# Performance work log

Hardware: AMD Instinct MI355X
Metric: run time of the kernel (lower is better)

## Reference

```python
import jax, jax.numpy as jnp
import numpy as np

HEADS, OUT_CH = 8, 32  # GATConv(128, 256//8, heads=8) -> concat width 256
NEG_SLOPE = 0.2


def setup_inputs() -> dict:
    key = jax.random.key(0)
    ks = jax.random.split(key, 12)
    N, E, F_IN = 50000, 500000, 128
    H, C = HEADS, OUT_CH
    HID = H * C            # 256
    x = jax.random.normal(ks[0], (N, F_IN), dtype=jnp.float32)
    edge_index = jax.random.randint(ks[1], (2, E), 0, N, dtype=jnp.int64)
    s = 1.0 / np.sqrt(F_IN)
    W_gat = jax.random.normal(ks[2], (F_IN, H * C), dtype=jnp.float32) * s
    att_src = jax.random.normal(ks[3], (H, C), dtype=jnp.float32) * (1.0 / np.sqrt(C))
    att_dst = jax.random.normal(ks[4], (H, C), dtype=jnp.float32) * (1.0 / np.sqrt(C))
    b_gat = jnp.zeros((HID,), dtype=jnp.float32)
    W1 = jax.random.normal(ks[5], (HID, HID // 2), dtype=jnp.float32) * (1.0 / np.sqrt(HID))
    b1 = jnp.zeros((HID // 2,), dtype=jnp.float32)
    W2 = jax.random.normal(ks[6], (HID // 2, 6), dtype=jnp.float32) * (1.0 / np.sqrt(HID // 2))
    b2 = jnp.zeros((6,), dtype=jnp.float32)
    return {"x": x, "edge_index": edge_index, "W_gat": W_gat, "att_src": att_src,
            "att_dst": att_dst, "b_gat": b_gat, "W1": W1, "b1": b1, "W2": W2, "b2": b2}


def _gat_forward(x, edge_index, W_gat, att_src, att_dst, b_gat):
    N = x.shape[0]
    H, C = HEADS, OUT_CH
    # add self loops (PyG GATConv default)
    loop = jnp.arange(N, dtype=edge_index.dtype)
    src = jnp.concatenate([edge_index[0], loop])
    dst = jnp.concatenate([edge_index[1], loop])
    # per-node transform: [N, H, C]
    xh = (x @ W_gat).reshape(N, H, C)
    a_src = jnp.einsum('nhc,hc->nh', xh, att_src)  # [N, H]
    a_dst = jnp.einsum('nhc,hc->nh', xh, att_dst)  # [N, H]
    alpha = a_src[src] + a_dst[dst]                # [Etot, H]
    alpha = jnp.where(alpha >= 0, alpha, NEG_SLOPE * alpha)  # leaky relu
    # segment softmax over destination nodes
    m = jax.ops.segment_max(alpha, dst, num_segments=N)     # [N, H]
    m = jax.lax.stop_gradient(m)
    ex = jnp.exp(alpha - m[dst])
    denom = jax.ops.segment_sum(ex, dst, num_segments=N)    # [N, H]
    coef = ex / denom[dst]                                   # [Etot, H]
    # weighted scatter-add aggregation
    msgs = xh[src] * coef[:, :, None]                        # [Etot, H, C]
    out = jax.ops.segment_sum(msgs, dst, num_segments=N)     # [N, H, C]
    return out.reshape(N, H * C) + b_gat


def reference(x, edge_index, W_gat, att_src, att_dst, b_gat, W1, b1, W2, b2):
    h = _gat_forward(x, edge_index, W_gat, att_src, att_dst, b_gat)
    h = jax.nn.elu(h)
    g = jnp.mean(h, axis=0, keepdims=True)   # [1, 256] mean pool
    g = jax.nn.relu(g @ W1 + b1)
    return g @ W2 + b2                        # [1, 6] logits
```

## Files before the change

kernel.cpp:

```cpp
#include <hip/hip_runtime.h>
#include <hip/hip_fp8.h>
#include <math.h>

#define F_IN 128
#define HID 256
#define NH 8
#define CAP 40
#define BCAP 4096

typedef _Float16 h16;
typedef __attribute__((ext_vector_type(8))) _Float16 half8;
typedef __attribute__((ext_vector_type(4))) float f32x4;

__device__ inline unsigned char f32_to_fp8(float v) {
#if __has_builtin(__builtin_amdgcn_cvt_pk_fp8_f32)
    return (unsigned char)(__builtin_amdgcn_cvt_pk_fp8_f32(v, v, 0, false) & 0xff);
#else
    __hip_fp8_e4m3 t(v);
    return (unsigned char)t.__x;
#endif
}

__device__ inline void fp8x4_to_f32(int w, float* out) {
#if __has_builtin(__builtin_amdgcn_cvt_pk_f32_fp8)
    auto lo = __builtin_amdgcn_cvt_pk_f32_fp8(w, false);
    auto hi = __builtin_amdgcn_cvt_pk_f32_fp8(w, true);
    out[0] = lo[0]; out[1] = lo[1]; out[2] = hi[0]; out[3] = hi[1];
#else
    #pragma unroll
    for (int k = 0; k < 4; ++k) {
        __hip_fp8_e4m3 t;
        t.__x = (unsigned char)((w >> (8 * k)) & 0xff);
        out[k] = (float)t;
    }
#endif
}

__global__ void k_prep(const float* __restrict__ Wg, h16* __restrict__ Wt_sw,
                       int* gcur, float* g2, int n) {
    int i = blockIdx.x * 256 + threadIdx.x;
    if (i < 256) gcur[i] = 0;
    if (i < 256 * HID) g2[i] = 0.f;
    if (i < 4096) {
        int fid = i;
        int lane16 = fid & 15;
        int quad = (fid >> 4) & 3;
        int ks = (fid >> 6) & 3;
        int ct = fid >> 8;
        int col = ct * 16 + lane16;
        int k0 = ks * 32 + quad * 8;
        half8 v;
        #pragma unroll
        for (int j = 0; j < 8; ++j) v[j] = (h16)Wg[(size_t)(k0 + j) * HID + col];
        *(half8*)(Wt_sw + (size_t)fid * 8) = v;
    }
}

__global__ __launch_bounds__(256) void k_part(const int* __restrict__ dstp,
                                              const int* __restrict__ srcp,
                                              unsigned int* __restrict__ gbuck,
                                              int* __restrict__ gcur,
                                              int e, int nbuck) {
    __shared__ int hist[256];
    __shared__ int base[256];
    __shared__ int cur[256];
    int t = threadIdx.x;
    int c0 = blockIdx.x * 4096;
    hist[t] = 0;
    __syncthreads();
    #pragma unroll
    for (int j = 0; j < 16; ++j) {
        int i = c0 + j * 256 + t;
        if (i < e) atomicAdd(&hist[dstp[i] >> 8], 1);
    }
    __syncthreads();
    if (t < nbuck && hist[t] > 0) base[t] = atomicAdd(&gcur[t], hist[t]);
    cur[t] = 0;
    __syncthreads();
    #pragma unroll
    for (int j = 0; j < 16; ++j) {
        int i = c0 + j * 256 + t;
        if (i < e) {
            int d = dstp[i];
            int b = d >> 8;
            int pos = base[b] + atomicAdd(&cur[b], 1);
            if (pos < BCAP)
                gbuck[(size_t)b * BCAP + pos] =
                    ((unsigned)(d & 255) << 16) | (unsigned)srcp[i];
        }
    }
}

__global__ __launch_bounds__(256) void k_bin(const unsigned int* __restrict__ gbuck,
                                             const int* __restrict__ gcur,
                                             int* __restrict__ cnt,
                                             unsigned short* __restrict__ bin,
                                             int n, int nbuck) {
    __shared__ int hist[256];
    __shared__ int cur[256];
    __shared__ __align__(16) unsigned short bl[256 * CAP];
    int t = threadIdx.x;
    int b = blockIdx.x;
    int count = gcur[b];
    if (count > BCAP) count = BCAP;
    hist[t] = 0;
    __syncthreads();
    const unsigned int* bb = gbuck + (size_t)b * BCAP;
    for (int j = t; j < count; j += 256) atomicAdd(&hist[(bb[j] >> 16) & 255], 1);
    __syncthreads();
    int node = b * 256 + t;
    if (node < n) {
        int hh = hist[t];
        cnt[node] = hh > CAP ? CAP : hh;
    }
    cur[t] = 0;
    __syncthreads();
    for (int j = t; j < count; j += 256) {
        unsigned int wv = bb[j];
        int dl = (wv >> 16) & 255;
        int pos = atomicAdd(&cur[dl], 1);
        if (pos < CAP) bl[dl * CAP + pos] = (unsigned short)(wv & 0xffff);
    }
    __syncthreads();
    const int4* s4 = (const int4*)bl;
    int4* d4 = (int4*)(bin + (size_t)b * 256 * CAP);
    #pragma unroll
    for (int q = 0; q < 5; ++q) d4[q * 256 + t] = s4[q * 256 + t];
}

__global__ __launch_bounds__(512) void k_gemm(const float* __restrict__ x,
                                              const h16* __restrict__ Wt_sw,
                                              const float* __restrict__ att_s,
                                              const float* __restrict__ att_d,
                                              unsigned char* __restrict__ xh8,
                                              float* __restrict__ a_src,
                                              float* __restrict__ a_dst,
                                              int n, int ntiles) {
    __shared__ h16 wlds[32768];
    int t = threadIdx.x;
    int w = t >> 6, l = t & 63;
    int lane16 = l & 15, quad = l >> 4;

    float4 pv0[4], pv1[4];
    int tile = blockIdx.x * 8 + w;
    bool have = tile < ntiles;
    int row0 = tile * 16;
    if (have) {
        int rA = row0 + lane16;
        if (rA >= n) rA = n - 1;
        const float* xrow = x + (size_t)rA * F_IN + quad * 8;
        #pragma unroll
        for (int ks = 0; ks < 4; ++ks) {
            pv0[ks] = *(const float4*)(xrow + ks * 32);
            pv1[ks] = *(const float4*)(xrow + ks * 32 + 4);
        }
    }
    {
        const int4* wsrc = (const int4*)Wt_sw;
        int4* wdst = (int4*)wlds;
        #pragma unroll
        for (int i = 0; i < 8; ++i) wdst[i * 512 + t] = wsrc[i * 512 + t];
    }
    __syncthreads();
    if (!have) return;
    const h16* wl = wlds + (size_t)l * 8;

    half8 afr[4];
    #pragma unroll
    for (int ks = 0; ks < 4; ++ks) {
        half8 a;
        a[0] = (h16)pv0[ks].x; a[1] = (h16)pv0[ks].y;
        a[2] = (h16)pv0[ks].z; a[3] = (h16)pv0[ks].w;
        a[4] = (h16)pv1[ks].x; a[5] = (h16)pv1[ks].y;
        a[6] = (h16)pv1[ks].z; a[7] = (h16)pv1[ks].w;
        afr[ks] = a;
    }
    f32x4 acc[16];
    #pragma unroll
    for (int ct = 0; ct < 16; ++ct) acc[ct] = (f32x4){0.f, 0.f, 0.f, 0.f};
    #pragma unroll
    for (int ct = 0; ct < 16; ++ct) {
        #pragma unroll
        for (int ks = 0; ks < 4; ++ks) {
            half8 bfr = *(const half8*)(wl + (ct * 4 + ks) * 512);
            acc[ct] = __builtin_amdgcn_mfma_f32_16x16x32_f16(afr[ks], bfr, acc[ct], 0, 0, 0);
        }
    }
    if (row0 + 16 <= n) {
        #pragma unroll
        for (int ct = 0; ct < 16; ++ct) {
            int col = ct * 16 + lane16;
            #pragma unroll
            for (int r = 0; r < 4; ++r)
                xh8[(size_t)(row0 + quad * 4 + r) * HID + col] = f32_to_fp8(acc[ct][r]);
        }
    } else {
        #pragma unroll
        for (int ct = 0; ct < 16; ++ct) {
            int col = ct * 16 + lane16;
            #pragma unroll
            for (int r = 0; r < 4; ++r) {
                int row = row0 + quad * 4 + r;
                if (row < n) xh8[(size_t)row * HID + col] = f32_to_fp8(acc[ct][r]);
            }
        }
    }
    #pragma unroll
    for (int h = 0; h < 8; ++h) {
        float ps[4] = {0.f, 0.f, 0.f, 0.f};
        float pd[4] = {0.f, 0.f, 0.f, 0.f};
        #pragma unroll
        for (int cc = 0; cc < 2; ++cc) {
            int ct = h * 2 + cc;
            float as_ = att_s[ct * 16 + lane16];
            float ad_ = att_d[ct * 16 + lane16];
            #pragma unroll
            for (int r = 0; r < 4; ++r) {
                ps[r] += acc[ct][r] * as_;
                pd[r] += acc[ct][r] * ad_;
            }
        }
        #pragma unroll
        for (int m = 1; m < 16; m <<= 1) {
            #pragma unroll
            for (int r = 0; r < 4; ++r) {
                ps[r] += __shfl_xor(ps[r], m, 64);
                pd[r] += __shfl_xor(pd[r], m, 64);
            }
        }
        if (lane16 == 0) {
            #pragma unroll
            for (int r = 0; r < 4; ++r) {
                int row = row0 + quad * 4 + r;
                if (row < n) {
                    a_src[row * NH + h] = ps[r];
                    a_dst[row * NH + h] = pd[r];
                }
            }
        }
    }
}

__global__ __launch_bounds__(256) void k_agg(const unsigned char* __restrict__ xh8,
                                             const float* __restrict__ a_src,
                                             const float* __restrict__ a_dst,
                                             const int* __restrict__ cnt,
                                             const unsigned short* __restrict__ bin,
                                             const float* __restrict__ b_gat,
                                             float* __restrict__ g2, int n) {
    __shared__ float wpart[4][260];
    int t = threadIdx.x;
    int slot = t >> 4;
    int cl = t & 15;
    int c0 = cl * 16;
    int h = cl >> 1;
    int nn = blockIdx.x * 16 + slot;
    bool alive = nn < n;
    int nnc = alive ? nn : (n - 1);

    float ad = a_dst[nnc * NH + h];
    int deg = cnt[nnc];
    if (deg > CAP) deg = CAP;

    float al = a_src[nnc * NH + h] + ad;
    al = al > 0.f ? al : 0.2f * al;
    float ex = __expf(al);
    float den = ex;
    float acc[16];
    {
        int4 v = *(const int4*)(xh8 + (size_t)nnc * HID + c0);
        float f[16];
        fp8x4_to_f32(v.x, f); fp8x4_to_f32(v.y, f + 4);
        fp8x4_to_f32(v.z, f + 8); fp8x4_to_f32(v.w, f + 12);
        #pragma unroll
        for (int i = 0; i < 16; ++i) acc[i] = ex * f[i];
    }
    const unsigned short* brow = bin + (size_t)nnc * CAP;
    int j = 0;
    for (; j + 4 <= deg; j += 4) {
        ushort4 ss = *(const ushort4*)(brow + j);
        int s0 = ss.x, s1 = ss.y, s2 = ss.z, s3 = ss.w;
        float aa[4];
        aa[0] = a_src[s0 * NH + h];
        aa[1] = a_src[s1 * NH + h];
        aa[2] = a_src[s2 * NH + h];
        aa[3] = a_src[s3 * NH + h];
        int4 v0 = *(const int4*)(xh8 + (size_t)s0 * HID + c0);
        int4 v1 = *(const int4*)(xh8 + (size_t)s1 * HID + c0);
        int4 v2 = *(const int4*)(xh8 + (size_t)s2 * HID + c0);
        int4 v3 = *(const int4*)(xh8 + (size_t)s3 * HID + c0);
        float e4[4];
        #pragma unroll
        for (int q = 0; q < 4; ++q) {
            float a2 = aa[q] + ad;
            a2 = a2 > 0.f ? a2 : 0.2f * a2;
            e4[q] = __expf(a2);
            den += e4[q];
        }
        float f[16];
        fp8x4_to_f32(v0.x, f); fp8x4_to_f32(v0.y, f + 4);
        fp8x4_to_f32(v0.z, f + 8); fp8x4_to_f32(v0.w, f + 12);
        #pragma unroll
        for (int i = 0; i < 16; ++i) acc[i] += e4[0] * f[i];
        fp8x4_to_f32(v1.x, f); fp8x4_to_f32(v1.y, f + 4);
        fp8x4_to_f32(v1.z, f + 8); fp8x4_to_f32(v1.w, f + 12);
        #pragma unroll
        for (int i = 0; i < 16; ++i) acc[i] += e4[1] * f[i];
        fp8x4_to_f32(v2.x, f); fp8x4_to_f32(v2.y, f + 4);
        fp8x4_to_f32(v2.z, f + 8); fp8x4_to_f32(v2.w, f + 12);
        #pragma unroll
        for (int i = 0; i < 16; ++i) acc[i] += e4[2] * f[i];
        fp8x4_to_f32(v3.x, f); fp8x4_to_f32(v3.y, f + 4);
        fp8x4_to_f32(v3.z, f + 8); fp8x4_to_f32(v3.w, f + 12);
        #pragma unroll
        for (int i = 0; i < 16; ++i) acc[i] += e4[3] * f[i];
    }
    for (; j < deg; ++j) {
        int s = brow[j];
        float a2 = a_src[s * NH + h] + ad;
        a2 = a2 > 0.f ? a2 : 0.2f * a2;
        float e2 = __expf(a2);
        den += e2;
        int4 v = *(const int4*)(xh8 + (size_t)s * HID + c0);
        float f[16];
        fp8x4_to_f32(v.x, f); fp8x4_to_f32(v.y, f + 4);
        fp8x4_to_f32(v.z, f + 8); fp8x4_to_f32(v.w, f + 12);
        #pragma unroll
        for (int i = 0; i < 16; ++i) acc[i] += e2 * f[i];
    }
    float inv = 1.f / den;
    float val[16];
    #pragma unroll
    for (int q = 0; q < 4; ++q) {
        float4 bv = *(const float4*)(b_gat + c0 + q * 4);
        val[q * 4 + 0] = acc[q * 4 + 0] * inv + bv.x;
        val[q * 4 + 1] = acc[q * 4 + 1] * inv + bv.y;
        val[q * 4 + 2] = acc[q * 4 + 2] * inv + bv.z;
        val[q * 4 + 3] = acc[q * 4 + 3] * inv + bv.w;
    }
    #pragma unroll
    for (int i = 0; i < 16; ++i) {
        float v = val[i];
        v = v > 0.f ? v : expm1f(v);
        val[i] = alive ? v : 0.f;
    }
    #pragma unroll
    for (int i = 0; i < 16; ++i) {
        val[i] += __shfl_xor(val[i], 16, 64);
        val[i] += __shfl_xor(val[i], 32, 64);
    }
    int w = t >> 6, lw = t & 63;
    if (lw < 16) {
        #pragma unroll
        for (int q = 0; q < 4; ++q)
            *(f32x4*)(&wpart[w][c0 + q * 4]) =
                (f32x4){val[q * 4], val[q * 4 + 1], val[q * 4 + 2], val[q * 4 + 3]};
    }
    __syncthreads();
    float s = wpart[0][t] + wpart[1][t] + wpart[2][t] + wpart[3][t];
    atomicAdd(&g2[(blockIdx.x & 255) * HID + t], s);
}

__global__ __launch_bounds__(256) void k_mlp(const float* __restrict__ g2,
                                             const float* __restrict__ W1,
                                             const float* __restrict__ b1,
                                             const float* __restrict__ W2,
                                             const float* __restrict__ b2,
                                             float* __restrict__ out, int n) {
    __shared__ float gm[HID];
    __shared__ float h1p[2][128];
    __shared__ float h1[128];
    int t = threadIdx.x;
    float s = 0.f;
    for (int b = 0; b < 256; ++b) s += g2[b * HID + t];
    gm[t] = s / (float)n;
    __syncthreads();
    int o = t & 127, hf = t >> 7;
    float a = 0.f;
    #pragma unroll 4
    for (int k = hf * 128; k < hf * 128 + 128; ++k) a += gm[k] * W1[k * 128 + o];
    h1p[hf][o] = a;
    __syncthreads();
    if (t < 128) {
        float v = h1p[0][t] + h1p[1][t] + b1[t];
        h1[t] = v > 0.f ? v : 0.f;
    }
    __syncthreads();
    if (t < 6) {
        float a2 = b2[t];
        for (int k = 0; k < 128; ++k) a2 += h1[k] * W2[k * 6 + t];
        out[t] = a2;
    }
}

extern "C" void kernel_launch(void* const* d_in, const int* in_sizes, int n_in,
                              void* d_out, int out_size, void* d_ws, size_t ws_size,
                              hipStream_t stream) {
    const float* x     = (const float*)d_in[0];
    const int*   ei    = (const int*)d_in[1];
    const float* Wg    = (const float*)d_in[2];
    const float* att_s = (const float*)d_in[3];
    const float* att_d = (const float*)d_in[4];
    const float* b_gat = (const float*)d_in[5];
    const float* W1    = (const float*)d_in[6];
    const float* b1    = (const float*)d_in[7];
    const float* W2    = (const float*)d_in[8];
    const float* b2    = (const float*)d_in[9];

    int N = in_sizes[0] / F_IN;
    int E = in_sizes[1] / 2;
    const int* srcp = ei;
    const int* dstp = ei + E;
    int nblk = (N + 15) / 16;
    int ntiles = (N + 15) / 16;
    int nbuck = (N + 255) >> 8;

    char* ws = (char*)d_ws;
    size_t off = 0;
    auto alloc = [&](size_t bytes) {
        size_t o = off;
        off += (bytes + 255) & ~(size_t)255;
        return o;
    };
    unsigned char* xh8 = (unsigned char*)(ws + alloc((size_t)N * HID));
    h16*   Wt      = (h16*)(ws + alloc((size_t)F_IN * HID * 2));
    float* asr     = (float*)(ws + alloc((size_t)N * NH * 4));
    float* ads     = (float*)(ws + alloc((size_t)N * NH * 4));
    int*   cnt     = (int*)(ws + alloc((size_t)N * 4));
    unsigned short* bin = (unsigned short*)(ws + alloc((size_t)nbuck * 256 * CAP * 2));
    float* g2      = (float*)(ws + alloc((size_t)256 * HID * 4));
    unsigned int* gbuck = (unsigned int*)(ws + alloc((size_t)nbuck * BCAP * 4));
    int*   gcur    = (int*)(ws + alloc((size_t)256 * 4));

    int nb1 = (E + 4095) / 4096;
    int ngemm = (ntiles + 7) / 8;

    k_prep<<<256, 256, 0, stream>>>(Wg, Wt, gcur, g2, N);
    k_part<<<nb1, 256, 0, stream>>>(dstp, srcp, gbuck, gcur, E, nbuck);
    k_bin<<<nbuck, 256, 0, stream>>>(gbuck, gcur, cnt, bin, N, nbuck);
    k_gemm<<<ngemm, 512, 0, stream>>>(x, Wt, att_s, att_d, xh8, asr, ads, N, ntiles);
    k_agg<<<nblk, 256, 0, stream>>>(xh8, asr, ads, cnt, bin, b_gat, g2, N);
    k_mlp<<<1, 256, 0, stream>>>(g2, W1, b1, W2, b2, (float*)d_out, N);
}
```

Measured before the change: 188.7 us.

## Merge edge partition and node GEMM into one launch, locally sort edges per bucket

Replaces the separate partition and GEMM kernels with a single launch whose first blocks partition edges and whose remaining blocks run the MFMA GEMM. The two independent stages can then overlap, and one kernel launch and its tail are removed. The partition path also sorts each chunk by bucket in shared memory, using a prefix scan, before writing, so global bucket writes become contiguous runs instead of scattered stores. The cost is 64KB of LDS per block for both roles, which may lower occupancy for the partition blocks, plus extra barriers for the scan.

```diff
diff --git a/kernel.cpp b/kernel.cpp
--- a/kernel.cpp
+++ b/kernel.cpp
@@ -56,37 +56,185 @@
     }
 }
 
-__global__ __launch_bounds__(256) void k_part(const int* __restrict__ dstp,
-                                              const int* __restrict__ srcp,
-                                              unsigned int* __restrict__ gbuck,
-                                              int* __restrict__ gcur,
-                                              int e, int nbuck) {
-    __shared__ int hist[256];
-    __shared__ int base[256];
-    __shared__ int cur[256];
+__global__ __launch_bounds__(512) void k_ga(const float* __restrict__ x,
+                                            const h16* __restrict__ Wt_sw,
+                                            const float* __restrict__ att_s,
+                                            const float* __restrict__ att_d,
+                                            const int* __restrict__ dstp,
+                                            const int* __restrict__ srcp,
+                                            unsigned char* __restrict__ xh8,
+                                            float* __restrict__ a_src,
+                                            float* __restrict__ a_dst,
+                                            unsigned int* __restrict__ gbuck,
+                                            int* __restrict__ gcur,
+                                            int n, int e, int ntiles,
+                                            int nbuck, int npart) {
+    __shared__ __align__(16) char smem[65536];
     int t = threadIdx.x;
-    int c0 = blockIdx.x * 4096;
-    hist[t] = 0;
-    __syncthreads();
-    #pragma unroll
-    for (int j = 0; j < 16; ++j) {
-        int i = c0 + j * 256 + t;
-        if (i < e) atomicAdd(&hist[dstp[i] >> 8], 1);
-    }
-    __syncthreads();
-    if (t < nbuck && hist[t] > 0) base[t] = atomicAdd(&gcur[t], hist[t]);
-    cur[t] = 0;
-    __syncthreads();
-    #pragma unroll
-    for (int j = 0; j < 16; ++j) {
-        int i = c0 + j * 256 + t;
-        if (i < e) {
-            int d = dstp[i];
-            int b = d >> 8;
-            int pos = base[b] + atomicAdd(&cur[b], 1);
-            if (pos < BCAP)
-                gbuck[(size_t)b * BCAP + pos] =
-                    ((unsigned)(d & 255) << 16) | (unsigned)srcp[i];
+
+    if (blockIdx.x < (unsigned)npart) {
+        int* hist  = (int*)smem;
+        int* scn   = hist + 256;
+        int* lbase = scn + 256;
+        int* lcur  = lbase + 256;
+        int* base  = lcur + 256;
+        unsigned int* sorted = (unsigned int*)(base + 256);
+        int c0 = blockIdx.x * 4096;
+
+        if (t < 256) hist[t] = 0;
+        __syncthreads();
+
+        unsigned int w8[8];
+        int b8[8];
+        #pragma unroll
+        for (int k = 0; k < 8; ++k) {
+            int i = c0 + k * 512 + t;
+            if (i < e) {
+                int d = dstp[i];
+                int s = srcp[i];
+                int b = d >> 8;
+                b8[k] = b;
+                w8[k] = ((unsigned)b << 24) | ((unsigned)(d & 255) << 16) | (unsigned)s;
+                atomicAdd(&hist[b], 1);
+            } else {
+                b8[k] = -1;
+                w8[k] = 0;
+            }
+        }
+        __syncthreads();
+        if (t < 256) scn[t] = hist[t];
+        __syncthreads();
+        for (int off = 1; off < 256; off <<= 1) {
+            int u = 0;
+            if (t < 256 && t >= off) u = scn[t - off];
+            __syncthreads();
+            if (t < 256 && t >= off) scn[t] += u;
+            __syncthreads();
+        }
+        if (t < 256) {
+            lbase[t] = scn[t] - hist[t];
+            lcur[t] = 0;
+            if (t < nbuck && hist[t] > 0) base[t] = atomicAdd(&gcur[t], hist[t]);
+        }
+        __syncthreads();
+        #pragma unroll
+        for (int k = 0; k < 8; ++k) {
+            if (b8[k] >= 0) {
+                int r = atomicAdd(&lcur[b8[k]], 1);
+                sorted[lbase[b8[k]] + r] = w8[k];
+            }
+        }
+        __syncthreads();
+        int total = scn[255];
+        for (int j = t; j < total; j += 512) {
+            unsigned int w = sorted[j];
+            int b = w >> 24;
+            int addr = base[b] + (j - lbase[b]);
+            if (addr < BCAP) gbuck[(size_t)b * BCAP + addr] = w;
+        }
+        return;
+    }
+
+    h16* wlds = (h16*)smem;
+    int w = t >> 6, l = t & 63;
+    int lane16 = l & 15, quad = l >> 4;
+
+    float4 pv0[4], pv1[4];
+    int tile = (blockIdx.x - npart) * 8 + w;
+    bool have = tile < ntiles;
+    int row0 = tile * 16;
+    if (have) {
+        int rA = row0 + lane16;
+        if (rA >= n) rA = n - 1;
+        const float* xrow = x + (size_t)rA * F_IN + quad * 8;
+        #pragma unroll
+        for (int ks = 0; ks < 4; ++ks) {
+            pv0[ks] = *(const float4*)(xrow + ks * 32);
+            pv1[ks] = *(const float4*)(xrow + ks * 32 + 4);
+        }
+    }
+    {
+        const int4* wsrc = (const int4*)Wt_sw;
+        int4* wdst = (int4*)wlds;
+        #pragma unroll
+        for (int i = 0; i < 8; ++i) wdst[i * 512 + t] = wsrc[i * 512 + t];
+    }
+    __syncthreads();
+    if (!have) return;
+    const h16* wl = wlds + (size_t)l * 8;
+
+    half8 afr[4];
+    #pragma unroll
+    for (int ks = 0; ks < 4; ++ks) {
+        half8 a;
+        a[0] = (h16)pv0[ks].x; a[1] = (h16)pv0[ks].y;
+        a[2] = (h16)pv0[ks].z; a[3] = (h16)pv0[ks].w;
+        a[4] = (h16)pv1[ks].x; a[5] = (h16)pv1[ks].y;
+        a[6] = (h16)pv1[ks].z; a[7] = (h16)pv1[ks].w;
+        afr[ks] = a;
+    }
+    f32x4 acc[16];
+    #pragma unroll
+    for (int ct = 0; ct < 16; ++ct) acc[ct] = (f32x4){0.f, 0.f, 0.f, 0.f};
+    #pragma unroll
+    for (int ct = 0; ct < 16; ++ct) {
+        #pragma unroll
+        for (int ks = 0; ks < 4; ++ks) {
+            half8 bfr = *(const half8*)(wl + (ct * 4 + ks) * 512);
+            acc[ct] = __builtin_amdgcn_mfma_f32_16x16x32_f16(afr[ks], bfr, acc[ct], 0, 0, 0);
+        }
+    }
+    if (row0 + 16 <= n) {
+        #pragma unroll
+        for (int ct = 0; ct < 16; ++ct) {
+            int col = ct * 16 + lane16;
+            #pragma unroll
+            for (int r = 0; r < 4; ++r)
+                xh8[(size_t)(row0 + quad * 4 + r) * HID + col] = f32_to_fp8(acc[ct][r]);
+        }
+    } else {
+        #pragma unroll
+        for (int ct = 0; ct < 16; ++ct) {
+            int col = ct * 16 + lane16;
+            #pragma unroll
+            for (int r = 0; r < 4; ++r) {
+                int row = row0 + quad * 4 + r;
+                if (row < n) xh8[(size_t)row * HID + col] = f32_to_fp8(acc[ct][r]);
+            }
+        }
+    }
+    #pragma unroll
+    for (int h = 0; h < 8; ++h) {
+        float ps[4] = {0.f, 0.f, 0.f, 0.f};
+        float pd[4] = {0.f, 0.f, 0.f, 0.f};
+        #pragma unroll
+        for (int cc = 0; cc < 2; ++cc) {
+            int ct = h * 2 + cc;
+            float as_ = att_s[ct * 16 + lane16];
+            float ad_ = att_d[ct * 16 + lane16];
+            #pragma unroll
+            for (int r = 0; r < 4; ++r) {
+                ps[r] += acc[ct][r] * as_;
+                pd[r] += acc[ct][r] * ad_;
+            }
+        }
+        #pragma unroll
+        for (int m = 1; m < 16; m <<= 1) {
+            #pragma unroll
+            for (int r = 0; r < 4; ++r) {
+                ps[r] += __shfl_xor(ps[r], m, 64);
+                pd[r] += __shfl_xor(pd[r], m, 64);
+            }
+        }
+        if (lane16 == 0) {
+            #pragma unroll
+            for (int r = 0; r < 4; ++r) {
+                int row = row0 + quad * 4 + r;
+                if (row < n) {
+                    a_src[row * NH + h] = ps[r];
+                    a_dst[row * NH + h] = pd[r];
+                }
+            }
         }
     }
 }
@@ -126,119 +274,6 @@
     int4* d4 = (int4*)(bin + (size_t)b * 256 * CAP);
     #pragma unroll
     for (int q = 0; q < 5; ++q) d4[q * 256 + t] = s4[q * 256 + t];
-}
-
-__global__ __launch_bounds__(512) void k_gemm(const float* __restrict__ x,
-                                              const h16* __restrict__ Wt_sw,
-                                              const float* __restrict__ att_s,
-                                              const float* __restrict__ att_d,
-                                              unsigned char* __restrict__ xh8,
-                                              float* __restrict__ a_src,
-                                              float* __restrict__ a_dst,
-                                              int n, int ntiles) {
-    __shared__ h16 wlds[32768];
-    int t = threadIdx.x;
-    int w = t >> 6, l = t & 63;
-    int lane16 = l & 15, quad = l >> 4;
-
-    float4 pv0[4], pv1[4];
-    int tile = blockIdx.x * 8 + w;
-    bool have = tile < ntiles;
-    int row0 = tile * 16;
-    if (have) {
-        int rA = row0 + lane16;
-        if (rA >= n) rA = n - 1;
-        const float* xrow = x + (size_t)rA * F_IN + quad * 8;
-        #pragma unroll
-        for (int ks = 0; ks < 4; ++ks) {
-            pv0[ks] = *(const float4*)(xrow + ks * 32);
-            pv1[ks] = *(const float4*)(xrow + ks * 32 + 4);
-        }
-    }
-    {
-        const int4* wsrc = (const int4*)Wt_sw;
-        int4* wdst = (int4*)wlds;
-        #pragma unroll
-        for (int i = 0; i < 8; ++i) wdst[i * 512 + t] = wsrc[i * 512 + t];
-    }
-    __syncthreads();
-    if (!have) return;
-    const h16* wl = wlds + (size_t)l * 8;
-
-    half8 afr[4];
-    #pragma unroll
-    for (int ks = 0; ks < 4; ++ks) {
-        half8 a;
-        a[0] = (h16)pv0[ks].x; a[1] = (h16)pv0[ks].y;
-        a[2] = (h16)pv0[ks].z; a[3] = (h16)pv0[ks].w;
-        a[4] = (h16)pv1[ks].x; a[5] = (h16)pv1[ks].y;
-        a[6] = (h16)pv1[ks].z; a[7] = (h16)pv1[ks].w;
-        afr[ks] = a;
-    }
-    f32x4 acc[16];
-    #pragma unroll
-    for (int ct = 0; ct < 16; ++ct) acc[ct] = (f32x4){0.f, 0.f, 0.f, 0.f};
-    #pragma unroll
-    for (int ct = 0; ct < 16; ++ct) {
-        #pragma unroll
-        for (int ks = 0; ks < 4; ++ks) {
-            half8 bfr = *(const half8*)(wl + (ct * 4 + ks) * 512);
-            acc[ct] = __builtin_amdgcn_mfma_f32_16x16x32_f16(afr[ks], bfr, acc[ct], 0, 0, 0);
-        }
-    }
-    if (row0 + 16 <= n) {
-        #pragma unroll
-        for (int ct = 0; ct < 16; ++ct) {
-            int col = ct * 16 + lane16;
-            #pragma unroll
-            for (int r = 0; r < 4; ++r)
-                xh8[(size_t)(row0 + quad * 4 + r) * HID + col] = f32_to_fp8(acc[ct][r]);
-        }
-    } else {
-        #pragma unroll
-        for (int ct = 0; ct < 16; ++ct) {
-            int col = ct * 16 + lane16;
-            #pragma unroll
-            for (int r = 0; r < 4; ++r) {
-                int row = row0 + quad * 4 + r;
-                if (row < n) xh8[(size_t)row * HID + col] = f32_to_fp8(acc[ct][r]);
-            }
-        }
-    }
-    #pragma unroll
-    for (int h = 0; h < 8; ++h) {
-        float ps[4] = {0.f, 0.f, 0.f, 0.f};
-        float pd[4] = {0.f, 0.f, 0.f, 0.f};
-        #pragma unroll
-        for (int cc = 0; cc < 2; ++cc) {
-            int ct = h * 2 + cc;
-            float as_ = att_s[ct * 16 + lane16];
-            float ad_ = att_d[ct * 16 + lane16];
-            #pragma unroll
-            for (int r = 0; r < 4; ++r) {
-                ps[r] += acc[ct][r] * as_;
-                pd[r] += acc[ct][r] * ad_;
-            }
-        }
-        #pragma unroll
-        for (int m = 1; m < 16; m <<= 1) {
-            #pragma unroll
-            for (int r = 0; r < 4; ++r) {
-                ps[r] += __shfl_xor(ps[r], m, 64);
-                pd[r] += __shfl_xor(pd[r], m, 64);
-            }
-        }
-        if (lane16 == 0) {
-            #pragma unroll
-            for (int r = 0; r < 4; ++r) {
-                int row = row0 + quad * 4 + r;
-                if (row < n) {
-                    a_src[row * NH + h] = ps[r];
-                    a_dst[row * NH + h] = pd[r];
-                }
-            }
-        }
-    }
 }
 
 __global__ __launch_bounds__(256) void k_agg(const unsigned char* __restrict__ xh8,
@@ -432,13 +467,14 @@
     unsigned int* gbuck = (unsigned int*)(ws + alloc((size_t)nbuck * BCAP * 4));
     int*   gcur    = (int*)(ws + alloc((size_t)256 * 4));
 
-    int nb1 = (E + 4095) / 4096;
+    int npart = (E + 4095) / 4096;
     int ngemm = (ntiles + 7) / 8;
 
     k_prep<<<256, 256, 0, stream>>>(Wg, Wt, gcur, g2, N);
-    k_part<<<nb1, 256, 0, stream>>>(dstp, srcp, gbuck, gcur, E, nbuck);
+    k_ga<<<npart + ngemm, 512, 0, stream>>>(x, Wt, att_s, att_d, dstp, srcp,
+                                            xh8, asr, ads, gbuck, gcur,
+                                            N, E, ntiles, nbuck, npart);
     k_bin<<<nbuck, 256, 0, stream>>>(gbuck, gcur, cnt, bin, N, nbuck);
-    k_gemm<<<ngemm, 512, 0, stream>>>(x, Wt, att_s, att_d, xh8, asr, ads, N, ntiles);
     k_agg<<<nblk, 256, 0, stream>>>(xh8, asr, ads, cnt, bin, b_gat, g2, N);
     k_mlp<<<1, 256, 0, stream>>>(g2, W1, b1, W2, b2, (float*)d_out, N);
 }
```

Result: faster. 175.2 us (-7.1%).
